# Optimization experiments

Hardware: AMD Instinct MI355X
Metric: run time of the kernel (lower is better)

## Reference

```python
import jax, jax.numpy as jnp
import numpy as np

# Dims: batch B, seq L, embed D, router hidden H, num_blocks NB, top_k K
B, L, D, H, NB, K = 8, 4096, 1024, 64, 16, 2
TEMP = 2.0          # current_temperature buffer (init 2.0), clamp(min=0.1) inert
LN_EPS = 1e-5


def setup_inputs() -> dict:
    key = jax.random.key(0)
    k_x, k_w1, k_w2 = jax.random.split(key, 3)
    return {
        "x": jax.random.normal(k_x, (B, L, D), dtype=jnp.float32),
        "ln_gamma": jnp.ones((D,), dtype=jnp.float32),
        "ln_beta": jnp.zeros((D,), dtype=jnp.float32),
        "W1": jax.random.normal(k_w1, (D, H), dtype=jnp.float32) / np.sqrt(D).astype(np.float32),
        "W2": jax.random.normal(k_w2, (H, NB), dtype=jnp.float32) / np.sqrt(H).astype(np.float32),
    }


def reference(x, ln_gamma, ln_beta, W1, W2):
    # gate: LayerNorm -> Linear(no bias) -> GELU(exact) -> Linear(no bias)
    mu = jnp.mean(x, axis=-1, keepdims=True)
    var = jnp.mean(jnp.square(x - mu), axis=-1, keepdims=True)
    xn = (x - mu) * jax.lax.rsqrt(var + LN_EPS) * ln_gamma + ln_beta
    h = jax.nn.gelu(xn @ W1, approximate=False)          # (B, L, H)
    logits = (h @ W2) / TEMP                              # (B, L, NB)

    probs = jax.nn.softmax(logits, axis=-1)               # (B, L, NB)
    top_probs, indices = jax.lax.top_k(probs, K)          # (B, L, K) each
    weights = top_probs / (jnp.sum(top_probs, axis=-1, keepdims=True) + 1e-8)

    # load-balancing aux loss: f = fraction of assignments per block (detached),
    # P = mean router prob per block
    counts = jnp.zeros((NB,), dtype=probs.dtype).at[indices.reshape(-1)].add(1.0)
    f = jax.lax.stop_gradient(counts) / (B * L * K + 1e-8)
    P = jnp.mean(probs, axis=(0, 1))                      # (NB,)
    aux_loss = NB * jnp.sum(f * P)

    return probs, indices, aux_loss, weights
```

## Files before the change

kernel.cpp:

```cpp
#include <hip/hip_runtime.h>
#include <math.h>

#define NTOK 32768
#define DDIM 1024
#define HDIM 64
#define NB 16
#define LN_EPS 1e-5f


__global__ void colsum_kernel(const float* __restrict__ W1,
                              const float* __restrict__ gamma,
                              const float* __restrict__ beta,
                              float* ws) {
    __shared__ float sg[4][64];
    __shared__ float sb[4][64];
    const int t = threadIdx.x;
    const int j = t & 63;
    const int part = t >> 6;
    const int d0 = blockIdx.x * 64 + part * 16;
    float ag = 0.f, ab = 0.f;
    for (int dd = 0; dd < 16; ++dd) {
        const int d = d0 + dd;
        const float w = W1[d * HDIM + j];
        ag += gamma[d] * w;
        ab += beta[d] * w;
    }
    sg[part][j] = ag;
    sb[part][j] = ab;
    __syncthreads();
    if (t < 64) {
        atomicAdd(&ws[32 + t], sg[0][t] + sg[1][t] + sg[2][t] + sg[3][t]);
        atomicAdd(&ws[96 + t], sb[0][t] + sb[1][t] + sb[2][t] + sb[3][t]);
    }
}

__global__ __launch_bounds__(256, 2)
void router_main(const float* __restrict__ x,
                 const float* __restrict__ gamma,
                 const float* __restrict__ W1,
                 const float* __restrict__ W2,
                 float* ws,
                 float* __restrict__ out) {
    __shared__ __align__(16) float Asub[32][64];
    __shared__ __align__(16) float Bsub[32][64];
    __shared__ __align__(16) float W2t[16][68];
    __shared__ float csgl[64], csbl[64];
    __shared__ float s1l[64], s2l[64];
    __shared__ __align__(16) float ylds[64][64];
    __shared__ __align__(16) float plds[64][16];
    __shared__ __align__(16) float ilds[128];
    __shared__ __align__(16) float wlds[128];
    __shared__ float cntl[16];

    const int t = threadIdx.x;
    const int blk = blockIdx.x;
    const int tok0 = blk * 64;

    if (t < 64) {
        for (int i = 0; i < 16; ++i) W2t[i][t] = W2[t * NB + i];
        csgl[t] = ws[32 + t];
        csbl[t] = ws[96 + t];
    }
    if (t >= 64 && t < 80) cntl[t - 64] = 0.f;

    const int tx = t & 15, ty = t >> 4;
    const int m0 = ty * 4, j0 = tx * 4;
    float acc[4][4] = {};
    float s1a = 0.f, s2a = 0.f, s1b = 0.f, s2b = 0.f;

    const int arow = t >> 3;
    const int acol = (t & 7) * 4;
    const int bkk  = t >> 4;
    const int bj   = (t & 15) * 4;

    for (int kc = 0; kc < 32; ++kc) {
        const int k0 = kc * 32;
        const float4 av0 = *(const float4*)&x[(size_t)(tok0 + arow) * DDIM + k0 + acol];
        const float4 av1 = *(const float4*)&x[(size_t)(tok0 + 32 + arow) * DDIM + k0 + acol];
        const float4 gv  = *(const float4*)&gamma[k0 + acol];
        const float4 bv0 = *(const float4*)&W1[(size_t)(k0 + bkk) * HDIM + bj];
        const float4 bv1 = *(const float4*)&W1[(size_t)(k0 + 16 + bkk) * HDIM + bj];
        __syncthreads();

        s1a += av0.x + av0.y + av0.z + av0.w;
        s2a += av0.x * av0.x + av0.y * av0.y + av0.z * av0.z + av0.w * av0.w;
        s1b += av1.x + av1.y + av1.z + av1.w;
        s2b += av1.x * av1.x + av1.y * av1.y + av1.z * av1.z + av1.w * av1.w;

        Asub[acol + 0][arow] = av0.x * gv.x;
        Asub[acol + 1][arow] = av0.y * gv.y;
        Asub[acol + 2][arow] = av0.z * gv.z;
        Asub[acol + 3][arow] = av0.w * gv.w;
        Asub[acol + 0][32 + arow] = av1.x * gv.x;
        Asub[acol + 1][32 + arow] = av1.y * gv.y;
        Asub[acol + 2][32 + arow] = av1.z * gv.z;
        Asub[acol + 3][32 + arow] = av1.w * gv.w;
        *(float4*)&Bsub[bkk][bj] = bv0;
        *(float4*)&Bsub[16 + bkk][bj] = bv1;
        __syncthreads();

#pragma unroll
        for (int kk = 0; kk < 32; ++kk) {
            const float4 a = *(const float4*)&Asub[kk][m0];
            const float4 b = *(const float4*)&Bsub[kk][j0];
            const float aa[4] = {a.x, a.y, a.z, a.w};
            const float bb[4] = {b.x, b.y, b.z, b.w};
#pragma unroll
            for (int i = 0; i < 4; ++i)
#pragma unroll
                for (int j = 0; j < 4; ++j)
                    acc[i][j] += aa[i] * bb[j];
        }
    }

#pragma unroll
    for (int i = 0; i < 4; ++i) {
        float4 v;
        v.x = acc[i][0]; v.y = acc[i][1]; v.z = acc[i][2]; v.w = acc[i][3];
        *(float4*)&ylds[m0 + i][j0] = v;
    }
#pragma unroll
    for (int msk = 1; msk <= 4; msk <<= 1) {
        s1a += __shfl_xor(s1a, msk, 64);
        s2a += __shfl_xor(s2a, msk, 64);
        s1b += __shfl_xor(s1b, msk, 64);
        s2b += __shfl_xor(s2b, msk, 64);
    }
    if ((t & 7) == 0) {
        s1l[arow] = s1a; s2l[arow] = s2a;
        s1l[32 + arow] = s1b; s2l[32 + arow] = s2b;
    }
    __syncthreads();

    const int em = t >> 2, eq = t & 3;
    const float mu = s1l[em] * (1.0f / 1024.0f);
    const float var = s2l[em] * (1.0f / 1024.0f) - mu * mu;
    const float rstd = 1.0f / sqrtf(var + LN_EPS);
#pragma unroll
    for (int jj = 0; jj < 16; ++jj) {
        const int j = eq * 16 + ((jj + em) & 15);
        const float y = ylds[em][j];
        const float pre = rstd * (y - mu * csgl[j]) + csbl[j];
        ylds[em][j] = 0.5f * pre * (1.0f + erff(pre * 0.70710678118654752f));
    }
    __syncthreads();

    float l[4] = {0.f, 0.f, 0.f, 0.f};
    for (int jj = 0; jj < 64; ++jj) {
        const int j = (jj + em) & 63;
        const float h = ylds[em][j];
#pragma unroll
        for (int c = 0; c < 4; ++c) l[c] += h * W2t[eq * 4 + c][j];
    }
#pragma unroll
    for (int c = 0; c < 4; ++c) plds[em][eq * 4 + c] = l[c] * 0.5f;
    __syncthreads();

    if (t < 64) {
        float p[16];
        float mx = -1e30f;
#pragma unroll
        for (int i = 0; i < NB; ++i) { p[i] = plds[t][i]; mx = fmaxf(mx, p[i]); }
        float s = 0.f;
#pragma unroll
        for (int i = 0; i < NB; ++i) { p[i] = expf(p[i] - mx); s += p[i]; }
        const float inv = 1.0f / s;
#pragma unroll
        for (int i = 0; i < NB; ++i) { p[i] *= inv; plds[t][i] = p[i]; }
        float b0 = -1.f, b1 = -1.f;
        int i0 = 0, i1 = 0;
#pragma unroll
        for (int i = 0; i < NB; ++i) {
            if (p[i] > b0)      { b1 = b0; i1 = i0; b0 = p[i]; i0 = i; }
            else if (p[i] > b1) { b1 = p[i]; i1 = i; }
        }
        const float wsum = b0 + b1 + 1e-8f;
        ilds[t * 2] = (float)i0;
        ilds[t * 2 + 1] = (float)i1;
        wlds[t * 2] = b0 / wsum;
        wlds[t * 2 + 1] = b1 / wsum;
        atomicAdd(&cntl[i0], 1.0f);
        atomicAdd(&cntl[i1], 1.0f);
    }
    __syncthreads();

    *(float4*)&out[(size_t)tok0 * NB + t * 4] = *(const float4*)(&plds[0][0] + t * 4);
    if (t < 32)
        *(float4*)&out[(size_t)NTOK * NB + tok0 * 2 + t * 4] = *(const float4*)&ilds[t * 4];
    if (t < 128)
        out[(size_t)NTOK * NB + (size_t)NTOK * 2 + 1 + tok0 * 2 + t] = wlds[t];

    if (t < 16) {
        float ps = 0.f;
        for (int m = 0; m < 64; ++m) ps += plds[m][t];
        atomicAdd(&ws[16 + t], ps);
        atomicAdd(&ws[t], cntl[t]);
    }
}

__global__ void aux_kernel(const float* ws, float* out) {
    if (threadIdx.x == 0) {
        float a = 0.f;
        for (int i = 0; i < NB; ++i) {
            const float f = ws[i] / (65536.0f + 1e-8f);
            const float P = ws[16 + i] * (1.0f / 32768.0f);
            a += f * P;
        }
        out[(size_t)NTOK * NB + (size_t)NTOK * 2] = 16.0f * a;
    }
}

extern "C" void kernel_launch(void* const* d_in, const int* in_sizes, int n_in,
                              void* d_out, int out_size, void* d_ws, size_t ws_size,
                              hipStream_t stream) {
    const float* x     = (const float*)d_in[0];
    const float* gamma = (const float*)d_in[1];
    const float* beta  = (const float*)d_in[2];
    const float* W1    = (const float*)d_in[3];
    const float* W2    = (const float*)d_in[4];
    float* out = (float*)d_out;
    float* ws  = (float*)d_ws;

    hipMemsetAsync(ws, 0, 160 * sizeof(float), stream);
    colsum_kernel<<<16, 256, 0, stream>>>(W1, gamma, beta, ws);
    router_main<<<NTOK / 64, 256, 0, stream>>>(x, gamma, W1, W2, ws, out);
    aux_kernel<<<1, 64, 0, stream>>>(ws, out);
}
```

Before: 257.2 us.

## Restructure router GEMM to per-wave column split with register prefetch and deterministic reductions

The main kernel now splits the 64 hidden columns across the four waves, 16 per wave. Each lane owns one token row and reads W1 values as wave-uniform scalar loads instead of staging them through shared memory. The next x chunk is prefetched into registers while the current one computes, and GELU plus the W2 projection run straight from registers with a cross-wave shared-memory reduction. The global atomics and memset are replaced by per-block partial sums that a wider aux kernel reduces. The catch is that each thread does more FMAs per A element and holds more registers, with less data reuse per shared-memory read.

```diff
diff --git a/kernel.cpp b/kernel.cpp
--- a/kernel.cpp
+++ b/kernel.cpp
@@ -7,11 +7,16 @@
 #define NB 16
 #define LN_EPS 1e-5f
 
+#define IDX_OFF  ((size_t)NTOK * NB)
+#define AUX_OFF  (IDX_OFF + (size_t)NTOK * 2)
+#define WT_OFF   (AUX_OFF + 1)
+
+#define WS_BLK 2048
 
 __global__ void colsum_kernel(const float* __restrict__ W1,
                               const float* __restrict__ gamma,
                               const float* __restrict__ beta,
-                              float* ws) {
+                              float* __restrict__ ws) {
     __shared__ float sg[4][64];
     __shared__ float sb[4][64];
     const int t = threadIdx.x;
@@ -29,8 +34,8 @@
     sb[part][j] = ab;
     __syncthreads();
     if (t < 64) {
-        atomicAdd(&ws[32 + t], sg[0][t] + sg[1][t] + sg[2][t] + sg[3][t]);
-        atomicAdd(&ws[96 + t], sb[0][t] + sb[1][t] + sb[2][t] + sb[3][t]);
+        ws[blockIdx.x * 64 + t]        = sg[0][t] + sg[1][t] + sg[2][t] + sg[3][t];
+        ws[1024 + blockIdx.x * 64 + t] = sb[0][t] + sb[1][t] + sb[2][t] + sb[3][t];
     }
 }
 
@@ -39,134 +44,136 @@
                  const float* __restrict__ gamma,
                  const float* __restrict__ W1,
                  const float* __restrict__ W2,
-                 float* ws,
+                 const float* __restrict__ cs,
+                 float* __restrict__ blkpart,
                  float* __restrict__ out) {
     __shared__ __align__(16) float Asub[32][64];
-    __shared__ __align__(16) float Bsub[32][64];
-    __shared__ __align__(16) float W2t[16][68];
-    __shared__ float csgl[64], csbl[64];
+    __shared__ float plds[4][64][17];
     __shared__ float s1l[64], s2l[64];
-    __shared__ __align__(16) float ylds[64][64];
-    __shared__ __align__(16) float plds[64][16];
-    __shared__ __align__(16) float ilds[128];
-    __shared__ __align__(16) float wlds[128];
-    __shared__ float cntl[16];
-
-    const int t = threadIdx.x;
-    const int blk = blockIdx.x;
-    const int tok0 = blk * 64;
-
-    if (t < 64) {
-        for (int i = 0; i < 16; ++i) W2t[i][t] = W2[t * NB + i];
-        csgl[t] = ws[32 + t];
-        csbl[t] = ws[96 + t];
-    }
-    if (t >= 64 && t < 80) cntl[t - 64] = 0.f;
-
-    const int tx = t & 15, ty = t >> 4;
-    const int m0 = ty * 4, j0 = tx * 4;
-    float acc[4][4] = {};
-    float s1a = 0.f, s2a = 0.f, s1b = 0.f, s2b = 0.f;
-
-    const int arow = t >> 3;
-    const int acol = (t & 7) * 4;
-    const int bkk  = t >> 4;
-    const int bj   = (t & 15) * 4;
+    __shared__ float cps[32];
+
+    const int t    = threadIdx.x;
+    const int lane = t & 63;
+    const int wv   = t >> 6;
+    const int tok0 = blockIdx.x * 64;
+
+    const int r  = t >> 2;
+    const int kq = t & 3;
+
+    const int jw = __builtin_amdgcn_readfirstlane(wv * 16);
+
+    float acc[16];
+#pragma unroll
+    for (int c = 0; c < 16; ++c) acc[c] = 0.f;
+    float s1p = 0.f, s2p = 0.f;
+
+    const float* xrow = x + (size_t)(tok0 + r) * DDIM;
+
+    float4 xa = *(const float4*)(xrow + kq * 4);
+    float4 xb = *(const float4*)(xrow + 16 + kq * 4);
+    float4 ga = *(const float4*)(gamma + kq * 4);
+    float4 gb = *(const float4*)(gamma + 16 + kq * 4);
+
+    if (t < 32) cps[t] = 0.f;
 
     for (int kc = 0; kc < 32; ++kc) {
         const int k0 = kc * 32;
-        const float4 av0 = *(const float4*)&x[(size_t)(tok0 + arow) * DDIM + k0 + acol];
-        const float4 av1 = *(const float4*)&x[(size_t)(tok0 + 32 + arow) * DDIM + k0 + acol];
-        const float4 gv  = *(const float4*)&gamma[k0 + acol];
-        const float4 bv0 = *(const float4*)&W1[(size_t)(k0 + bkk) * HDIM + bj];
-        const float4 bv1 = *(const float4*)&W1[(size_t)(k0 + 16 + bkk) * HDIM + bj];
+
+        s1p += xa.x + xa.y + xa.z + xa.w + xb.x + xb.y + xb.z + xb.w;
+        s2p += xa.x * xa.x + xa.y * xa.y + xa.z * xa.z + xa.w * xa.w
+             + xb.x * xb.x + xb.y * xb.y + xb.z * xb.z + xb.w * xb.w;
+
         __syncthreads();
 
-        s1a += av0.x + av0.y + av0.z + av0.w;
-        s2a += av0.x * av0.x + av0.y * av0.y + av0.z * av0.z + av0.w * av0.w;
-        s1b += av1.x + av1.y + av1.z + av1.w;
-        s2b += av1.x * av1.x + av1.y * av1.y + av1.z * av1.z + av1.w * av1.w;
-
-        Asub[acol + 0][arow] = av0.x * gv.x;
-        Asub[acol + 1][arow] = av0.y * gv.y;
-        Asub[acol + 2][arow] = av0.z * gv.z;
-        Asub[acol + 3][arow] = av0.w * gv.w;
-        Asub[acol + 0][32 + arow] = av1.x * gv.x;
-        Asub[acol + 1][32 + arow] = av1.y * gv.y;
-        Asub[acol + 2][32 + arow] = av1.z * gv.z;
-        Asub[acol + 3][32 + arow] = av1.w * gv.w;
-        *(float4*)&Bsub[bkk][bj] = bv0;
-        *(float4*)&Bsub[16 + bkk][bj] = bv1;
+        Asub[kq * 4 + 0][r] = xa.x * ga.x;
+        Asub[kq * 4 + 1][r] = xa.y * ga.y;
+        Asub[kq * 4 + 2][r] = xa.z * ga.z;
+        Asub[kq * 4 + 3][r] = xa.w * ga.w;
+        Asub[16 + kq * 4 + 0][r] = xb.x * gb.x;
+        Asub[16 + kq * 4 + 1][r] = xb.y * gb.y;
+        Asub[16 + kq * 4 + 2][r] = xb.z * gb.z;
+        Asub[16 + kq * 4 + 3][r] = xb.w * gb.w;
+
+        const int kn = (kc < 31) ? (k0 + 32) : 0;
+        float4 nxa = *(const float4*)(xrow + kn + kq * 4);
+        float4 nxb = *(const float4*)(xrow + kn + 16 + kq * 4);
+        float4 nga = *(const float4*)(gamma + kn + kq * 4);
+        float4 ngb = *(const float4*)(gamma + kn + 16 + kq * 4);
+
         __syncthreads();
 
+        const float* w1p = W1 + (size_t)k0 * HDIM + jw;
 #pragma unroll
         for (int kk = 0; kk < 32; ++kk) {
-            const float4 a = *(const float4*)&Asub[kk][m0];
-            const float4 b = *(const float4*)&Bsub[kk][j0];
-            const float aa[4] = {a.x, a.y, a.z, a.w};
-            const float bb[4] = {b.x, b.y, b.z, b.w};
-#pragma unroll
-            for (int i = 0; i < 4; ++i)
-#pragma unroll
-                for (int j = 0; j < 4; ++j)
-                    acc[i][j] += aa[i] * bb[j];
-        }
-    }
-
-#pragma unroll
-    for (int i = 0; i < 4; ++i) {
-        float4 v;
-        v.x = acc[i][0]; v.y = acc[i][1]; v.z = acc[i][2]; v.w = acc[i][3];
-        *(float4*)&ylds[m0 + i][j0] = v;
-    }
-#pragma unroll
-    for (int msk = 1; msk <= 4; msk <<= 1) {
-        s1a += __shfl_xor(s1a, msk, 64);
-        s2a += __shfl_xor(s2a, msk, 64);
-        s1b += __shfl_xor(s1b, msk, 64);
-        s2b += __shfl_xor(s2b, msk, 64);
-    }
-    if ((t & 7) == 0) {
-        s1l[arow] = s1a; s2l[arow] = s2a;
-        s1l[32 + arow] = s1b; s2l[32 + arow] = s2b;
-    }
-    __syncthreads();
-
-    const int em = t >> 2, eq = t & 3;
-    const float mu = s1l[em] * (1.0f / 1024.0f);
-    const float var = s2l[em] * (1.0f / 1024.0f) - mu * mu;
+            const float a = Asub[kk][lane];
+#pragma unroll
+            for (int c = 0; c < 16; ++c)
+                acc[c] = fmaf(a, w1p[kk * HDIM + c], acc[c]);
+        }
+
+        xa = nxa; xb = nxb; ga = nga; gb = ngb;
+    }
+
+    s1p += __shfl_xor(s1p, 1, 64);
+    s1p += __shfl_xor(s1p, 2, 64);
+    s2p += __shfl_xor(s2p, 1, 64);
+    s2p += __shfl_xor(s2p, 2, 64);
+    if ((t & 3) == 0) { s1l[r] = s1p; s2l[r] = s2p; }
+    __syncthreads();
+
+    const float mu   = s1l[lane] * (1.0f / 1024.0f);
+    const float var  = s2l[lane] * (1.0f / 1024.0f) - mu * mu;
     const float rstd = 1.0f / sqrtf(var + LN_EPS);
-#pragma unroll
-    for (int jj = 0; jj < 16; ++jj) {
-        const int j = eq * 16 + ((jj + em) & 15);
-        const float y = ylds[em][j];
-        const float pre = rstd * (y - mu * csgl[j]) + csbl[j];
-        ylds[em][j] = 0.5f * pre * (1.0f + erff(pre * 0.70710678118654752f));
-    }
-    __syncthreads();
-
-    float l[4] = {0.f, 0.f, 0.f, 0.f};
-    for (int jj = 0; jj < 64; ++jj) {
-        const int j = (jj + em) & 63;
-        const float h = ylds[em][j];
-#pragma unroll
-        for (int c = 0; c < 4; ++c) l[c] += h * W2t[eq * 4 + c][j];
-    }
-#pragma unroll
-    for (int c = 0; c < 4; ++c) plds[em][eq * 4 + c] = l[c] * 0.5f;
+
+    float csg[16], csb[16];
+#pragma unroll
+    for (int c = 0; c < 16; ++c) { csg[c] = 0.f; csb[c] = 0.f; }
+    for (int b = 0; b < 16; ++b) {
+#pragma unroll
+        for (int c = 0; c < 16; ++c) {
+            csg[c] += cs[b * 64 + jw + c];
+            csb[c] += cs[1024 + b * 64 + jw + c];
+        }
+    }
+
+#pragma unroll
+    for (int c = 0; c < 16; ++c) {
+        const float pre = rstd * (acc[c] - mu * csg[c]) + csb[c];
+        acc[c] = 0.5f * pre * (1.0f + erff(pre * 0.70710678118654752f));
+    }
+
+    float lp[16];
+#pragma unroll
+    for (int nb = 0; nb < NB; ++nb) lp[nb] = 0.f;
+    for (int c = 0; c < 16; ++c) {
+        const float h = acc[c];
+        const float* w2r = W2 + (size_t)(jw + c) * NB;
+#pragma unroll
+        for (int nb = 0; nb < NB; ++nb) lp[nb] = fmaf(h, w2r[nb], lp[nb]);
+    }
+#pragma unroll
+    for (int nb = 0; nb < NB; ++nb) plds[wv][lane][nb] = lp[nb] * 0.5f;
     __syncthreads();
 
     if (t < 64) {
         float p[16];
         float mx = -1e30f;
 #pragma unroll
-        for (int i = 0; i < NB; ++i) { p[i] = plds[t][i]; mx = fmaxf(mx, p[i]); }
+        for (int i = 0; i < NB; ++i) {
+            p[i] = plds[0][t][i] + plds[1][t][i] + plds[2][t][i] + plds[3][t][i];
+            mx = fmaxf(mx, p[i]);
+        }
         float s = 0.f;
 #pragma unroll
         for (int i = 0; i < NB; ++i) { p[i] = expf(p[i] - mx); s += p[i]; }
         const float inv = 1.0f / s;
 #pragma unroll
-        for (int i = 0; i < NB; ++i) { p[i] *= inv; plds[t][i] = p[i]; }
+        for (int i = 0; i < NB; ++i) p[i] *= inv;
+
+        float* po = out + (size_t)(tok0 + t) * NB;
+#pragma unroll
+        for (int i = 0; i < NB; ++i) { po[i] = p[i]; plds[0][t][i] = p[i]; }
+
         float b0 = -1.f, b1 = -1.f;
         int i0 = 0, i1 = 0;
 #pragma unroll
@@ -175,38 +182,47 @@
             else if (p[i] > b1) { b1 = p[i]; i1 = i; }
         }
         const float wsum = b0 + b1 + 1e-8f;
-        ilds[t * 2] = (float)i0;
-        ilds[t * 2 + 1] = (float)i1;
-        wlds[t * 2] = b0 / wsum;
-        wlds[t * 2 + 1] = b1 / wsum;
-        atomicAdd(&cntl[i0], 1.0f);
-        atomicAdd(&cntl[i1], 1.0f);
-    }
-    __syncthreads();
-
-    *(float4*)&out[(size_t)tok0 * NB + t * 4] = *(const float4*)(&plds[0][0] + t * 4);
-    if (t < 32)
-        *(float4*)&out[(size_t)NTOK * NB + tok0 * 2 + t * 4] = *(const float4*)&ilds[t * 4];
-    if (t < 128)
-        out[(size_t)NTOK * NB + (size_t)NTOK * 2 + 1 + tok0 * 2 + t] = wlds[t];
+        out[IDX_OFF + (size_t)(tok0 + t) * 2]     = (float)i0;
+        out[IDX_OFF + (size_t)(tok0 + t) * 2 + 1] = (float)i1;
+        out[WT_OFF + (size_t)(tok0 + t) * 2]      = b0 / wsum;
+        out[WT_OFF + (size_t)(tok0 + t) * 2 + 1]  = b1 / wsum;
+        atomicAdd(&cps[i0], 1.0f);
+        atomicAdd(&cps[i1], 1.0f);
+    }
+    __syncthreads();
 
     if (t < 16) {
         float ps = 0.f;
-        for (int m = 0; m < 64; ++m) ps += plds[m][t];
-        atomicAdd(&ws[16 + t], ps);
-        atomicAdd(&ws[t], cntl[t]);
-    }
-}
-
-__global__ void aux_kernel(const float* ws, float* out) {
-    if (threadIdx.x == 0) {
+        for (int m = 0; m < 64; ++m) ps += plds[0][m][t];
+        blkpart[(size_t)blockIdx.x * 32 + 16 + t] = ps;
+        blkpart[(size_t)blockIdx.x * 32 + t]      = cps[t];
+    }
+}
+
+__global__ void aux_kernel(const float* __restrict__ ws, float* __restrict__ out) {
+    __shared__ float red[8][32];
+    const int t = threadIdx.x;
+    const int i = t & 31;
+    const int part = t >> 5;
+    float s = 0.f;
+    for (int b = part; b < 512; b += 8) s += ws[WS_BLK + (size_t)b * 32 + i];
+    red[part][i] = s;
+    __syncthreads();
+    if (t < 32) {
+        float tot = 0.f;
+#pragma unroll
+        for (int pp = 0; pp < 8; ++pp) tot += red[pp][t];
+        red[0][t] = tot;
+    }
+    __syncthreads();
+    if (t == 0) {
         float a = 0.f;
-        for (int i = 0; i < NB; ++i) {
-            const float f = ws[i] / (65536.0f + 1e-8f);
-            const float P = ws[16 + i] * (1.0f / 32768.0f);
+        for (int i2 = 0; i2 < 16; ++i2) {
+            const float f = red[0][i2] / (65536.0f + 1e-8f);
+            const float P = red[0][16 + i2] * (1.0f / 32768.0f);
             a += f * P;
         }
-        out[(size_t)NTOK * NB + (size_t)NTOK * 2] = 16.0f * a;
+        out[AUX_OFF] = 16.0f * a;
     }
 }
 
@@ -221,8 +237,8 @@
     float* out = (float*)d_out;
     float* ws  = (float*)d_ws;
 
-    hipMemsetAsync(ws, 0, 160 * sizeof(float), stream);
     colsum_kernel<<<16, 256, 0, stream>>>(W1, gamma, beta, ws);
-    router_main<<<NTOK / 64, 256, 0, stream>>>(x, gamma, W1, W2, ws, out);
-    aux_kernel<<<1, 64, 0, stream>>>(ws, out);
-}
+    router_main<<<NTOK / 64, 256, 0, stream>>>(x, gamma, W1, W2,
+                                               ws, ws + WS_BLK, out);
+    aux_kernel<<<1, 256, 0, stream>>>(ws, out);
+}
```

Measured after the change: 279.8 us. +8.8%, slower.
